# Kernel tuning notes

Measured on AMD Instinct MI355X. Metric: run time of the kernel, lower is better.

Reference implementation:

```python
import jax, jax.numpy as jnp
import numpy as np

_W1 = np.array([[[-1, 0, 0], [0, 1, 0], [0, 0, 0]],
                [[0, -1, 0], [0, 1, 0], [0, 0, 0]],
                [[0, 0, -1], [0, 1, 0], [0, 0, 0]],
                [[0, 0, 0], [-1, 1, 0], [0, 0, 0]]], dtype=np.float32).reshape(4, 1, 3, 3)
_W2 = _W1[:, :, ::-1, ::-1].copy()

BN_EPS = 1e-3  # YOLOX BaseConv BatchNorm eps
SHIFTS = (1, 3)


def _conv1x1(x, w, b=None):
    # x: (B,C,H,W), w: (O,C,1,1)
    y = jnp.einsum('bchw,oc->bohw', x, w[:, :, 0, 0])
    if b is not None:
        y = y + b[None, :, None, None]
    return y


def _grouped_dilated(x, w, d, groups):
    # 3x3 grouped conv, dilation d, 'same' padding (pad = d for 3x3)
    return jax.lax.conv_general_dilated(
        x, w, window_strides=(1, 1), padding=((d, d), (d, d)),
        rhs_dilation=(d, d), dimension_numbers=('NCHW', 'OIHW', 'NCHW'),
        feature_group_count=groups)


def setup_inputs() -> dict:
    key = jax.random.key(0)
    ks = jax.random.split(key, 6)
    B, C, H, W = 4, 128, 384, 384
    Cq = C // 4
    return {
        'cen': jax.random.normal(ks[0], (B, C, H, W), jnp.float32),
        'mas': jax.random.normal(ks[1], (B, 1, H, W), jnp.float32),
        'scales': jnp.zeros((4,), jnp.float32),
        'in_conv_w': jax.random.normal(ks[2], (Cq, C, 1, 1), jnp.float32) * 0.05,
        'in_conv_b': jnp.zeros((Cq,), jnp.float32),
        'base_w': jax.random.normal(ks[3], (Cq, Cq, 1, 1), jnp.float32) * 0.1,
        'bn_gamma': jnp.ones((Cq,), jnp.float32),
        'bn_beta': jnp.zeros((Cq,), jnp.float32),
        'bn_mean': jnp.zeros((Cq,), jnp.float32),
        'bn_var': jnp.ones((Cq,), jnp.float32),
        'out_w': jax.random.normal(ks[4], (1, Cq, 1, 1), jnp.float32) * 0.1,
        'out_b': jnp.zeros((1,), jnp.float32),
    }


def reference(cen, mas, scales, in_conv_w, in_conv_b, base_w,
              bn_gamma, bn_beta, bn_mean, bn_var, out_w, out_b):
    B, C, H, W = cen.shape
    Cq = C // 4
    k1 = jnp.asarray(np.tile(_W1, (Cq, 1, 1, 1)))  # (4*Cq,1,3,3)
    k2 = jnp.asarray(np.tile(_W2, (Cq, 1, 1, 1)))

    x = _conv1x1(cen, in_conv_w, in_conv_b)  # (B,Cq,H,W)
    outs = []
    for shift in SHIFTS:
        o1 = _grouped_dilated(x, k1, shift, Cq)  # (B,4*Cq,H,W)
        o2 = _grouped_dilated(x, k2, shift, Cq)
        o = (o1 * o2).reshape(B, Cq, 4, H, W).min(axis=2)
        outs.append(o)
    outs = jnp.stack(outs, axis=-1)  # (B,Cq,H,W,n_shifts)
    feat = jax.nn.relu(outs.max(axis=-1) + outs.mean(axis=-1))

    # out_conv = BaseConv(1x1, BN, SiLU) + Conv2d(Cq->1, 1x1)
    y = _conv1x1(feat, base_w)
    inv = jax.lax.rsqrt(bn_var + BN_EPS)
    y = (y - bn_mean[None, :, None, None]) * (bn_gamma * inv)[None, :, None, None] + bn_beta[None, :, None, None]
    y = jax.nn.silu(y)
    att = jax.nn.sigmoid(_conv1x1(y, out_w, out_b))  # (B,1,H,W)

    s = jax.nn.softmax(scales)
    m = jax.nn.sigmoid(mas)
    return cen * (att * m * s[0] + m * s[1] + s[2] * att + s[3])
```

## Files before the change

kernel.cpp:

```cpp
#include <hip/hip_runtime.h>

#define HH 384
#define WW 384
#define HWSZ (HH*WW)
#define CIN 128
#define CQ 32
#define NB 4
#define NPIX (NB*HWSZ)

__device__ __forceinline__ float sigmoidf_(float v){ return 1.0f/(1.0f + __expf(-v)); }

__global__ __launch_bounds__(256) void k_prep(
    const float* __restrict__ in_w, const float* __restrict__ base_w,
    const float* __restrict__ bn_g, const float* __restrict__ bn_b,
    const float* __restrict__ bn_m, const float* __restrict__ bn_v,
    const float* __restrict__ out_w, const float* __restrict__ out_b,
    const float* __restrict__ scales,
    float* __restrict__ wt, float* __restrict__ bt, float* __restrict__ prm){
  int t = threadIdx.x;
  for (int i = t; i < CIN*CQ; i += 256){ int c = i >> 5, o = i & 31; wt[i] = in_w[o*CIN + c]; }
  for (int i = t; i < CQ*CQ;  i += 256){ int c = i >> 5, o = i & 31; bt[i] = base_w[o*CQ + c]; }
  if (t < CQ){
    float inv = rsqrtf(bn_v[t] + 1e-3f);
    float g = bn_g[t]*inv;
    prm[t]      = g;
    prm[32 + t] = bn_b[t] - bn_m[t]*g;
    prm[64 + t] = out_w[t];
  }
  if (t == 0){
    float s0=scales[0], s1=scales[1], s2=scales[2], s3=scales[3];
    float mx = fmaxf(fmaxf(s0,s1), fmaxf(s2,s3));
    float e0=expf(s0-mx), e1=expf(s1-mx), e2=expf(s2-mx), e3=expf(s3-mx);
    float inv = 1.0f/(e0+e1+e2+e3);
    prm[96]=e0*inv; prm[97]=e1*inv; prm[98]=e2*inv; prm[99]=e3*inv;
    prm[100]=out_b[0];
  }
}

__global__ __launch_bounds__(256) void k_conv1(const float* __restrict__ cen,
    const float* __restrict__ wt, const float* __restrict__ bvec,
    float* __restrict__ x) {
  int t = threadIdx.x;
  int p0  = blockIdx.x * 512 + t*2;
  int b   = p0 / HWSZ;
  int pix = p0 - b*HWSZ;
  const float* cb = cen + (size_t)b*CIN*HWSZ + pix;
  float2 acc[CQ];
  #pragma unroll
  for (int o=0;o<CQ;o++){ acc[o].x=0.f; acc[o].y=0.f; }
  #pragma unroll 2
  for (int c=0;c<CIN;c++){
    float2 v = *(const float2*)(cb + (size_t)c*HWSZ);
    const float* wc = wt + c*CQ;
    #pragma unroll
    for (int o=0;o<CQ;o++){
      float w = wc[o];
      acc[o].x = fmaf(v.x, w, acc[o].x);
      acc[o].y = fmaf(v.y, w, acc[o].y);
    }
  }
  float* xb = x + (size_t)b*CQ*HWSZ + pix;
  #pragma unroll
  for (int o=0;o<CQ;o++){
    float bb = bvec[o];
    float2 r; r.x = acc[o].x + bb; r.y = acc[o].y + bb;
    *(float2*)(xb + (size_t)o*HWSZ) = r;
  }
}

#define TH 8
#define TW 64
#define LDSW 72
#define LDSN (14*LDSW)
#define GBX 6
#define GBY 48

__device__ __forceinline__ float stencil_eval(const float* p){
  float xv = p[0];
  float q0 = (xv-p[-LDSW-1])*(xv-p[ LDSW+1]);
  float q1 = (xv-p[-LDSW  ])*(xv-p[ LDSW  ]);
  float q2 = (xv-p[-LDSW+1])*(xv-p[ LDSW-1]);
  float q3 = (xv-p[-1     ])*(xv-p[ 1     ]);
  float os0 = fminf(fminf(q0,q1),fminf(q2,q3));
  float r0 = (xv-p[-3*LDSW-3])*(xv-p[ 3*LDSW+3]);
  float r1 = (xv-p[-3*LDSW  ])*(xv-p[ 3*LDSW  ]);
  float r2 = (xv-p[-3*LDSW+3])*(xv-p[ 3*LDSW-3]);
  float r3 = (xv-p[-3      ])*(xv-p[ 3       ]);
  float os1 = fminf(fminf(r0,r1),fminf(r2,r3));
  float v = fmaxf(os0,os1) + 0.5f*(os0+os1);
  return fmaxf(v, 0.0f);
}

__global__ __launch_bounds__(256) void k_att(const float* __restrict__ x,
    const float* __restrict__ mas, const float* __restrict__ bt,
    const float* __restrict__ prm, float* __restrict__ a_out) {
  __shared__ float tile[2][LDSN];
  int t = threadIdx.x;

  int gid = blockIdx.x;
  int b   = gid / (GBX*GBY);
  int rem = gid - b*(GBX*GBY);
  int ty  = rem / GBX;
  int tx  = rem - ty*GBX;
  int h0  = ty*TH, w0 = tx*TW;

  int soff[4]; float sval[4];
  #pragma unroll
  for (int j=0;j<4;j++){
    int i = t + j*256;
    int r = i / LDSW, cc = i - r*LDSW;
    int hh = h0 - 3 + r, wq = w0 - 3 + cc;
    bool ok = (i < LDSN) && (cc < 70) &&
              ((unsigned)hh < (unsigned)HH) && ((unsigned)wq < (unsigned)WW);
    soff[j] = ok ? (hh*WW + wq) : 0;
    sval[j] = ok ? 1.0f : 0.0f;
  }

  int rr  = t >> 6, cc2 = t & 63;
  const int cbase0 = (3+rr)*LDSW + 3 + cc2;
  const int cbase1 = cbase0 + 4*LDSW;
  const float* xb = x + (size_t)b*CQ*HWSZ;

  float y0[CQ], y1[CQ];
  #pragma unroll
  for (int o=0;o<CQ;o++){ y0[o]=0.f; y1[o]=0.f; }

  #pragma unroll 2
  for (int c=0;c<CQ;c++){
    float* buf = tile[c&1];
    const float* xc = xb + (size_t)c*HWSZ;
    #pragma unroll
    for (int j=0;j<4;j++){
      int i = t + j*256;
      if (i < LDSN) buf[i] = sval[j] * xc[soff[j]];
    }
    __syncthreads();
    float fc0 = stencil_eval(buf + cbase0);
    float fc1 = stencil_eval(buf + cbase1);
    const float* wc = bt + c*CQ;
    #pragma unroll
    for (int o=0;o<CQ;o++){
      float w = wc[o];
      y0[o] = fmaf(fc0, w, y0[o]);
      y1[o] = fmaf(fc1, w, y1[o]);
    }
  }

  float w0p=prm[96], w1p=prm[97], w2p=prm[98], w3p=prm[99], ob=prm[100];
  float lin0=ob, lin1=ob;
  #pragma unroll
  for (int o=0;o<CQ;o++){
    float g=prm[o], sh=prm[32+o], ow=prm[64+o];
    float yy0 = fmaf(y0[o], g, sh);
    float yy1 = fmaf(y1[o], g, sh);
    lin0 = fmaf(ow*yy0, sigmoidf_(yy0), lin0);
    lin1 = fmaf(ow*yy1, sigmoidf_(yy1), lin1);
  }
  float att0 = sigmoidf_(lin0);
  float att1 = sigmoidf_(lin1);

  int pa = b*HWSZ + (h0+rr)*WW + (w0+cc2);
  int pc = pa + 4*WW;
  float m0 = sigmoidf_(mas[pa]);
  float m1 = sigmoidf_(mas[pc]);
  a_out[pa] = (att0*m0)*w0p + m0*w1p + att0*w2p + w3p;
  a_out[pc] = (att1*m1)*w0p + m1*w1p + att1*w2p + w3p;
}

__global__ __launch_bounds__(256) void k_out(const float* __restrict__ cen,
    const float* __restrict__ a, float* __restrict__ out){
  unsigned i = blockIdx.x*256u + threadIdx.x;
  unsigned e = i*4u;
  unsigned bc  = e / HWSZ;
  unsigned pix = e - bc*HWSZ;
  unsigned b   = bc >> 7;
  float4 v  = ((const float4*)cen)[i];
  float4 av = ((const float4*)a)[(b*HWSZ + pix) >> 2];
  float4 r;
  r.x = v.x*av.x; r.y = v.y*av.y; r.z = v.z*av.z; r.w = v.w*av.w;
  ((float4*)out)[i] = r;
}

extern "C" void kernel_launch(void* const* d_in, const int* in_sizes, int n_in,
                              void* d_out, int out_size, void* d_ws, size_t ws_size,
                              hipStream_t stream) {
  const float* cen    = (const float*)d_in[0];
  const float* mas    = (const float*)d_in[1];
  const float* scales = (const float*)d_in[2];
  const float* in_w   = (const float*)d_in[3];
  const float* in_b   = (const float*)d_in[4];
  const float* base_w = (const float*)d_in[5];
  const float* bn_g   = (const float*)d_in[6];
  const float* bn_b   = (const float*)d_in[7];
  const float* bn_m   = (const float*)d_in[8];
  const float* bn_v   = (const float*)d_in[9];
  const float* out_w  = (const float*)d_in[10];
  const float* out_b  = (const float*)d_in[11];
  float* out = (float*)d_out;

  float* x   = (float*)d_ws;
  float* a   = x  + (size_t)NB*CQ*HWSZ;
  float* wt  = a  + (size_t)NB*HWSZ;
  float* bt  = wt + (size_t)CIN*CQ;
  float* prm = bt + (size_t)CQ*CQ;

  k_prep <<<1, 256, 0, stream>>>(in_w, base_w, bn_g, bn_b, bn_m, bn_v,
                                 out_w, out_b, scales, wt, bt, prm);
  k_conv1<<<NPIX/512, 256, 0, stream>>>(cen, wt, in_b, x);
  k_att  <<<NB*GBX*GBY, 256, 0, stream>>>(x, mas, bt, prm, a);
  k_out  <<<(NB*CIN*HWSZ)/1024, 256, 0, stream>>>(cen, a, out);
}
```

Before: 698.4 us.

## Prefetch channel loads in conv1 and attention, pair adjacent pixels per thread

The 1x1 input conv now loads four channels ahead into registers so global loads overlap the FMA work, and folds the bias into the accumulator initialisation. The attention kernel prefetches the next channel's halo values into registers before the barrier. Each thread now handles two horizontally adjacent pixels instead of two pixels four rows apart. That lets the two stencils share float2 LDS reads and makes the mask load and output store vectorised. The cost is higher register pressure from the prefetch buffers, which could lower occupancy.

```diff
diff --git a/kernel.cpp b/kernel.cpp
--- a/kernel.cpp
+++ b/kernel.cpp
@@ -47,25 +47,33 @@
   const float* cb = cen + (size_t)b*CIN*HWSZ + pix;
   float2 acc[CQ];
   #pragma unroll
-  for (int o=0;o<CQ;o++){ acc[o].x=0.f; acc[o].y=0.f; }
-  #pragma unroll 2
-  for (int c=0;c<CIN;c++){
-    float2 v = *(const float2*)(cb + (size_t)c*HWSZ);
+  for (int o=0;o<CQ;o++){ float bb = bvec[o]; acc[o].x=bb; acc[o].y=bb; }
+
+  float2 cur[4], nxt[4];
+  #pragma unroll
+  for (int k=0;k<4;k++) cur[k] = *(const float2*)(cb + (size_t)k*HWSZ);
+
+  for (int c=0;c<CIN;c+=4){
+    if (c+4 < CIN){
+      #pragma unroll
+      for (int k=0;k<4;k++) nxt[k] = *(const float2*)(cb + (size_t)(c+4+k)*HWSZ);
+    }
     const float* wc = wt + c*CQ;
     #pragma unroll
-    for (int o=0;o<CQ;o++){
-      float w = wc[o];
-      acc[o].x = fmaf(v.x, w, acc[o].x);
-      acc[o].y = fmaf(v.y, w, acc[o].y);
-    }
+    for (int k=0;k<4;k++){
+      #pragma unroll
+      for (int o=0;o<CQ;o++){
+        float w = wc[k*CQ+o];
+        acc[o].x = fmaf(cur[k].x, w, acc[o].x);
+        acc[o].y = fmaf(cur[k].y, w, acc[o].y);
+      }
+    }
+    #pragma unroll
+    for (int k=0;k<4;k++) cur[k] = nxt[k];
   }
   float* xb = x + (size_t)b*CQ*HWSZ + pix;
   #pragma unroll
-  for (int o=0;o<CQ;o++){
-    float bb = bvec[o];
-    float2 r; r.x = acc[o].x + bb; r.y = acc[o].y + bb;
-    *(float2*)(xb + (size_t)o*HWSZ) = r;
-  }
+  for (int o=0;o<CQ;o++) *(float2*)(xb + (size_t)o*HWSZ) = acc[o];
 }
 
 #define TH 8
@@ -74,22 +82,6 @@
 #define LDSN (14*LDSW)
 #define GBX 6
 #define GBY 48
-
-__device__ __forceinline__ float stencil_eval(const float* p){
-  float xv = p[0];
-  float q0 = (xv-p[-LDSW-1])*(xv-p[ LDSW+1]);
-  float q1 = (xv-p[-LDSW  ])*(xv-p[ LDSW  ]);
-  float q2 = (xv-p[-LDSW+1])*(xv-p[ LDSW-1]);
-  float q3 = (xv-p[-1     ])*(xv-p[ 1     ]);
-  float os0 = fminf(fminf(q0,q1),fminf(q2,q3));
-  float r0 = (xv-p[-3*LDSW-3])*(xv-p[ 3*LDSW+3]);
-  float r1 = (xv-p[-3*LDSW  ])*(xv-p[ 3*LDSW  ]);
-  float r2 = (xv-p[-3*LDSW+3])*(xv-p[ 3*LDSW-3]);
-  float r3 = (xv-p[-3      ])*(xv-p[ 3       ]);
-  float os1 = fminf(fminf(r0,r1),fminf(r2,r3));
-  float v = fmaxf(os0,os1) + 0.5f*(os0+os1);
-  return fmaxf(v, 0.0f);
-}
 
 __global__ __launch_bounds__(256) void k_att(const float* __restrict__ x,
     const float* __restrict__ mas, const float* __restrict__ bt,
@@ -116,27 +108,81 @@
     sval[j] = ok ? 1.0f : 0.0f;
   }
 
-  int rr  = t >> 6, cc2 = t & 63;
-  const int cbase0 = (3+rr)*LDSW + 3 + cc2;
-  const int cbase1 = cbase0 + 4*LDSW;
+  int rr = t >> 5;
+  int ct = t & 31;
+  const int R = 3 + rr, C = 3 + 2*ct;
+  const int o_m3 = (R-3)*LDSW + C, o_m1 = (R-1)*LDSW + C,
+            o_0  =  R   *LDSW + C, o_p1 = (R+1)*LDSW + C,
+            o_p3 = (R+3)*LDSW + C;
   const float* xb = x + (size_t)b*CQ*HWSZ;
 
   float y0[CQ], y1[CQ];
   #pragma unroll
   for (int o=0;o<CQ;o++){ y0[o]=0.f; y1[o]=0.f; }
+
+  float rg[4];
+  #pragma unroll
+  for (int j=0;j<4;j++) rg[j] = xb[soff[j]];
 
   #pragma unroll 2
   for (int c=0;c<CQ;c++){
     float* buf = tile[c&1];
-    const float* xc = xb + (size_t)c*HWSZ;
     #pragma unroll
     for (int j=0;j<4;j++){
       int i = t + j*256;
-      if (i < LDSN) buf[i] = sval[j] * xc[soff[j]];
+      if (i < LDSN) buf[i] = sval[j]*rg[j];
+    }
+    float rg2[4];
+    if (c+1 < CQ){
+      const float* xn = xb + (size_t)(c+1)*HWSZ;
+      #pragma unroll
+      for (int j=0;j<4;j++) rg2[j] = xn[soff[j]];
     }
     __syncthreads();
-    float fc0 = stencil_eval(buf + cbase0);
-    float fc1 = stencil_eval(buf + cbase1);
+    const float* p = buf;
+    float2 m3a = *(const float2*)(p + o_m3 - 3);
+    float  m3b0 = p[o_m3], m3b1 = p[o_m3 + 1];
+    float2 m3c = *(const float2*)(p + o_m3 + 3);
+    float2 m1a = *(const float2*)(p + o_m1 - 1);
+    float2 m1b = *(const float2*)(p + o_m1 + 1);
+    float2 z0  = *(const float2*)(p + o_0  - 3);
+    float2 z1  = *(const float2*)(p + o_0  - 1);
+    float2 z2  = *(const float2*)(p + o_0  + 1);
+    float2 z3  = *(const float2*)(p + o_0  + 3);
+    float2 p1a = *(const float2*)(p + o_p1 - 1);
+    float2 p1b = *(const float2*)(p + o_p1 + 1);
+    float2 p3a = *(const float2*)(p + o_p3 - 3);
+    float  p3b0 = p[o_p3], p3b1 = p[o_p3 + 1];
+    float2 p3c = *(const float2*)(p + o_p3 + 3);
+
+    float xv = z1.y;
+    float q0 = (xv-m1a.x)*(xv-p1b.x);
+    float q1 = (xv-m1a.y)*(xv-p1a.y);
+    float q2 = (xv-m1b.x)*(xv-p1a.x);
+    float q3 = (xv-z1.x )*(xv-z2.x );
+    float os0 = fminf(fminf(q0,q1),fminf(q2,q3));
+    float r0 = (xv-m3a.x)*(xv-p3c.x);
+    float r1 = (xv-m3b0 )*(xv-p3b0 );
+    float r2 = (xv-m3c.x)*(xv-p3a.x);
+    float r3 = (xv-z0.x )*(xv-z3.x );
+    float os1 = fminf(fminf(r0,r1),fminf(r2,r3));
+    float v0 = fmaxf(os0,os1) + 0.5f*(os0+os1);
+    float fc0 = fmaxf(v0, 0.0f);
+
+    float xw = z2.x;
+    float u0 = (xw-m1a.y)*(xw-p1b.y);
+    float u1 = (xw-m1b.x)*(xw-p1b.x);
+    float u2 = (xw-m1b.y)*(xw-p1a.y);
+    float u3 = (xw-z1.y )*(xw-z2.y );
+    float ps0 = fminf(fminf(u0,u1),fminf(u2,u3));
+    float s0 = (xw-m3a.y)*(xw-p3c.y);
+    float s1 = (xw-m3b1 )*(xw-p3b1 );
+    float s2 = (xw-m3c.y)*(xw-p3a.y);
+    float s3 = (xw-z0.y )*(xw-z3.y );
+    float ps1 = fminf(fminf(s0,s1),fminf(s2,s3));
+    float v1 = fmaxf(ps0,ps1) + 0.5f*(ps0+ps1);
+    float fc1 = fmaxf(v1, 0.0f);
+
     const float* wc = bt + c*CQ;
     #pragma unroll
     for (int o=0;o<CQ;o++){
@@ -144,6 +190,8 @@
       y0[o] = fmaf(fc0, w, y0[o]);
       y1[o] = fmaf(fc1, w, y1[o]);
     }
+    #pragma unroll
+    for (int j=0;j<4;j++) rg[j] = rg2[j];
   }
 
   float w0p=prm[96], w1p=prm[97], w2p=prm[98], w3p=prm[99], ob=prm[100];
@@ -159,12 +207,14 @@
   float att0 = sigmoidf_(lin0);
   float att1 = sigmoidf_(lin1);
 
-  int pa = b*HWSZ + (h0+rr)*WW + (w0+cc2);
-  int pc = pa + 4*WW;
-  float m0 = sigmoidf_(mas[pa]);
-  float m1 = sigmoidf_(mas[pc]);
-  a_out[pa] = (att0*m0)*w0p + m0*w1p + att0*w2p + w3p;
-  a_out[pc] = (att1*m1)*w0p + m1*w1p + att1*w2p + w3p;
+  int pa = b*HWSZ + (h0+rr)*WW + (w0 + 2*ct);
+  float2 mm = *(const float2*)(mas + pa);
+  float m0 = sigmoidf_(mm.x);
+  float m1 = sigmoidf_(mm.y);
+  float2 res;
+  res.x = (att0*m0)*w0p + m0*w1p + att0*w2p + w3p;
+  res.y = (att1*m1)*w0p + m1*w1p + att1*w2p + w3p;
+  *(float2*)(a_out + pa) = res;
 }
 
 __global__ __launch_bounds__(256) void k_out(const float* __restrict__ cen,
```

Result: faster. 633.9 us (-9.2%).
